# Kernel tuning notes

Measured on AMD Instinct MI355X. Metric: run time of the kernel, lower is better.

Reference implementation:

```python
import jax, jax.numpy as jnp
import numpy as np

B, N = 8, 8192
EPS = 1e-8

def _linear(x, w, b):
    return x @ w.T + b

def _block(x, w1, b1, w2, b2):
    # BlockFC: Linear -> ReLU -> Linear -> ReLU
    return jax.nn.relu(_linear(jax.nn.relu(_linear(x, w1, b1)), w2, b2))

def _transform(pc_feat, img_feat, w, b):
    # AdaIN-style: normalize point features (unbiased var, torch.var default),
    # re-modulate with per-channel image mean/std, then Linear.
    pcn = (pc_feat - pc_feat.mean(-1, keepdims=True)) / jnp.sqrt(
        jnp.var(pc_feat, axis=-1, keepdims=True, ddof=1) + EPS)
    mean = img_feat.mean((2, 3))  # [B, C]
    var = jnp.var(img_feat.reshape(img_feat.shape[0], img_feat.shape[1], -1), axis=2, ddof=1)
    out = (pcn + mean[:, None, :]) * jnp.sqrt(var[:, None, :] + EPS)
    return _linear(out, w, b)

def _project(points, feat, proj_mat):
    # Perspective projection + bilinear gather of CNN features at point locations.
    Bb, Nn, _ = points.shape
    H, W = feat.shape[2], feat.shape[3]
    p4 = jnp.concatenate([points, jnp.ones((Bb, Nn, 1), points.dtype)], -1)
    coords = jnp.einsum('bij,bnj->bni', proj_mat, p4)  # [B, N, 4]
    x = (coords[..., 0] / coords[..., 3] + 1) / 2
    y = 1 - (coords[..., 1] / coords[..., 3] + 1) / 2
    x0 = jnp.clip(x * W, 0, W - 1)
    y0 = jnp.clip(y * H, 0, H - 1)
    x1f, x2f = jnp.floor(x0), jnp.ceil(x0)
    y1f, y2f = jnp.floor(y0), jnp.ceil(y0)
    xi1, xi2 = x1f.astype(jnp.int32), x2f.astype(jnp.int32)
    yi1, yi2 = y1f.astype(jnp.int32), y2f.astype(jnp.int32)
    ft = jnp.transpose(feat, (0, 3, 2, 1))  # [B, W, H, C], matches torch transpose(1, 3)
    bidx = jnp.arange(Bb)[:, None]
    Q11 = ft[bidx, xi1, yi1]
    Q12 = ft[bidx, xi1, yi2]
    Q21 = ft[bidx, xi2, yi1]
    Q22 = ft[bidx, xi2, yi2]
    return (((x2f - x0) * (y2f - y0))[..., None] * Q11
            + ((x0 - x1f) * (y2f - y0))[..., None] * Q21
            + ((x2f - x0) * (y0 - y1f))[..., None] * Q12
            + ((x0 - x1f) * (y0 - y1f))[..., None] * Q22)

def _forward(points, feat2, feat3, feat4, feat5, proj_mat,
             b0_w1, b0_b1, b0_w2, b0_b2, t0_w, t0_b,
             b1_w1, b1_b1, b1_w2, b1_b2, t1_w, t1_b,
             b2_w1, b2_b1, b2_w2, b2_b2, t2_w, t2_b,
             b3_w1, b3_b1, b3_w2, b3_b2, t3_w, t3_b,
             d1_w, d1_b, d2_w, d2_b, d3_w, d3_b, d4_w, d4_b):
    pc0 = _block(points, b0_w1, b0_b1, b0_w2, b0_b2)   # [B, N, 64]
    f0 = _transform(pc0, feat2, t0_w, t0_b)
    pc1 = _block(pc0, b1_w1, b1_b1, b1_w2, b1_b2)      # [B, N, 128]
    f1 = _transform(pc1, feat3, t1_w, t1_b)
    pc2 = _block(pc1, b2_w1, b2_b1, b2_w2, b2_b2)      # [B, N, 256]
    f2 = _transform(pc2, feat4, t2_w, t2_b)
    pc3 = _block(pc2, b3_w1, b3_b1, b3_w2, b3_b2)      # [B, N, 512]
    f3 = _transform(pc3, feat5, t3_w, t3_b)
    feats = jnp.concatenate([
        f0, f1, f2, f3,
        _project(points, feat2, proj_mat),
        _project(points, feat3, proj_mat),
        _project(points, feat4, proj_mat),
        _project(points, feat5, proj_mat),
        points], -1)                                   # [B, N, 1923]
    x = _linear(feats, d1_w, d1_b)
    x = _linear(jax.nn.relu(x), d2_w, d2_b)
    x = _linear(jax.nn.relu(x), d3_w, d3_b)
    x = _linear(jax.nn.relu(x), d4_w, d4_b)
    return x + points

def setup_inputs() -> dict:
    key = jax.random.key(0)
    ks = iter(jax.random.split(key, 80))
    d = {}
    d['points'] = jax.random.normal(next(ks), (B, N, 3), jnp.float32)
    d['feat2'] = jax.random.normal(next(ks), (B, 64, 112, 112), jnp.float32)
    d['feat3'] = jax.random.normal(next(ks), (B, 128, 56, 56), jnp.float32)
    d['feat4'] = jax.random.normal(next(ks), (B, 256, 28, 28), jnp.float32)
    d['feat5'] = jax.random.normal(next(ks), (B, 512, 14, 14), jnp.float32)
    d['proj_mat'] = jax.random.normal(next(ks), (B, 4, 4), jnp.float32)
    def linp(wn, bn, o, i):
        d[wn] = jax.random.normal(next(ks), (o, i), jnp.float32) / np.sqrt(i)
        d[bn] = jax.random.normal(next(ks), (o,), jnp.float32) * 0.01
    linp('b0_w1', 'b0_b1', 64, 3);   linp('b0_w2', 'b0_b2', 64, 64);   linp('t0_w', 't0_b', 64, 64)
    linp('b1_w1', 'b1_b1', 128, 64); linp('b1_w2', 'b1_b2', 128, 128); linp('t1_w', 't1_b', 128, 128)
    linp('b2_w1', 'b2_b1', 256, 128);linp('b2_w2', 'b2_b2', 256, 256); linp('t2_w', 't2_b', 256, 256)
    linp('b3_w1', 'b3_b1', 512, 256);linp('b3_w2', 'b3_b2', 512, 512); linp('t3_w', 't3_b', 512, 512)
    linp('d1_w', 'd1_b', 512, 1923); linp('d2_w', 'd2_b', 256, 512)
    linp('d3_w', 'd3_b', 128, 256);  linp('d4_w', 'd4_b', 3, 128)
    return d

def reference(points, feat2, feat3, feat4, feat5, proj_mat,
              b0_w1, b0_b1, b0_w2, b0_b2, t0_w, t0_b,
              b1_w1, b1_b1, b1_w2, b1_b2, t1_w, t1_b,
              b2_w1, b2_b1, b2_w2, b2_b2, t2_w, t2_b,
              b3_w1, b3_b1, b3_w2, b3_b2, t3_w, t3_b,
              d1_w, d1_b, d2_w, d2_b, d3_w, d3_b, d4_w, d4_b):
    return _forward(points, feat2, feat3, feat4, feat5, proj_mat,
                    b0_w1, b0_b1, b0_w2, b0_b2, t0_w, t0_b,
                    b1_w1, b1_b1, b1_w2, b1_b2, t1_w, t1_b,
                    b2_w1, b2_b1, b2_w2, b2_b2, t2_w, t2_b,
                    b3_w1, b3_b1, b3_w2, b3_b2, t3_w, t3_b,
                    d1_w, d1_b, d2_w, d2_b, d3_w, d3_b, d4_w, d4_b)
```

## Files before the change

### kernel.cpp

```cpp
#include <hip/hip_runtime.h>
#include <hip/hip_bf16.h>
#include <math.h>

#define BATCH   8
#define NPTS    8192
#define MTOT    (BATCH * NPTS)
#define EPSV    1e-8f

typedef __hip_bfloat16 bf16;
typedef __attribute__((ext_vector_type(8))) short short8;
typedef __attribute__((ext_vector_type(4))) float f32x4;

__global__ __launch_bounds__(256) void stats_kernel(
    const float* __restrict__ feat, int HW,
    float* __restrict__ mean, float* __restrict__ scale)
{
    int bc = blockIdx.x;
    const float* p = feat + (size_t)bc * HW;
    float s = 0.f, s2 = 0.f;
    for (int i = threadIdx.x; i < HW; i += 256) {
        float v = p[i];
        s += v; s2 += v * v;
    }
    for (int off = 32; off; off >>= 1) {
        s  += __shfl_xor(s,  off);
        s2 += __shfl_xor(s2, off);
    }
    __shared__ float shs[4], shs2[4];
    int wave = threadIdx.x >> 6, lane = threadIdx.x & 63;
    if (lane == 0) { shs[wave] = s; shs2[wave] = s2; }
    __syncthreads();
    if (threadIdx.x == 0) {
        float S  = shs[0] + shs[1] + shs[2] + shs[3];
        float S2 = shs2[0] + shs2[1] + shs2[2] + shs2[3];
        float m = S / HW;
        float var = (S2 - HW * m * m) / (HW - 1);
        mean[bc]  = m;
        scale[bc] = sqrtf(var + EPSV);
    }
}

__global__ __launch_bounds__(256) void fold_kernel(
    const float* __restrict__ A, int lda,
    const float* __restrict__ B, int ldb,
    bf16* __restrict__ Cc, int ldc, int N, int K)
{
    __shared__ float As[16][65];
    __shared__ float Bs[16][65];
    const int tid = threadIdx.x;
    const int m0 = blockIdx.x * 64;
    const int bn = blockIdx.y * 64;
    const int tx = tid & 15, ty = tid >> 4;
    float acc[4][4] = {};

    for (int k0 = 0; k0 < K; k0 += 16) {
        #pragma unroll
        for (int i = tid; i < 64 * 16; i += 256) {
            int r = i >> 4, k = i & 15;
            As[k][r] = A[(size_t)(m0 + r) * lda + k0 + k];
        }
        #pragma unroll
        for (int i = tid; i < 64 * 16; i += 256) {
            int n = i & 63, k = i >> 6;
            Bs[k][n] = B[(size_t)(k0 + k) * ldb + bn + n];
        }
        __syncthreads();
        #pragma unroll
        for (int kk = 0; kk < 16; ++kk) {
            float a[4], b[4];
            #pragma unroll
            for (int i = 0; i < 4; ++i) a[i] = As[kk][ty * 4 + i];
            #pragma unroll
            for (int j = 0; j < 4; ++j) b[j] = Bs[kk][tx * 4 + j];
            #pragma unroll
            for (int i = 0; i < 4; ++i)
                #pragma unroll
                for (int j = 0; j < 4; ++j)
                    acc[i][j] += a[i] * b[j];
        }
        __syncthreads();
    }
    #pragma unroll
    for (int i = 0; i < 4; ++i)
        #pragma unroll
        for (int j = 0; j < 4; ++j)
            Cc[(size_t)(m0 + ty * 4 + i) * ldc + bn + tx * 4 + j] =
                __float2bfloat16(acc[i][j]);
}

__global__ __launch_bounds__(64) void bias_all(
    const float* __restrict__ d1w, const float* __restrict__ d1b,
    const float* __restrict__ t0b, const float* __restrict__ t1b,
    const float* __restrict__ t2b, const float* __restrict__ t3b,
    float* __restrict__ out)
{
    int n = blockIdx.x;
    int lane = threadIdx.x;
    const float* row = d1w + (size_t)n * 1923;
    float s = 0.f;
    for (int k = lane; k < 960; k += 64) {
        float tv;
        if (k < 64)       tv = t0b[k];
        else if (k < 192) tv = t1b[k - 64];
        else if (k < 448) tv = t2b[k - 192];
        else              tv = t3b[k - 448];
        s += row[k] * tv;
    }
    for (int off = 32; off; off >>= 1) s += __shfl_xor(s, off);
    if (lane == 0) out[n] = d1b[n] + s;
}

struct ConvDesc { const float* src; bf16* dst; int srcLd, dstLd, rows, cols; };
struct ConvArgs { ConvDesc d[20]; int n; };

__global__ __launch_bounds__(256) void conv_batch(ConvArgs a)
{
    int di = blockIdx.y;
    if (di >= a.n) return;
    ConvDesc d = a.d[di];
    int total = d.rows * d.cols;
    for (int idx = blockIdx.x * 256 + threadIdx.x; idx < total;
         idx += gridDim.x * 256) {
        int r = idx / d.cols, c = idx % d.cols;
        float v = d.src ? d.src[(size_t)r * d.srcLd + c] : 0.f;
        d.dst[(size_t)r * d.dstLd + c] = __float2bfloat16(v);
    }
}

template<int BN>
__global__ __launch_bounds__(256) void gemm_bf16(
    const bf16* __restrict__ A, int lda,
    const bf16* __restrict__ W, int ldw,
    const float* __restrict__ bias,
    bf16* __restrict__ C, int ldc,
    int gx, int gy, int K)
{
    constexpr int LDK = 40;
    __shared__ __align__(16) bf16 As[128 * LDK];
    __shared__ __align__(16) bf16 Bs[BN * LDK];

    int nblk = gx * gy;
    int bid = blockIdx.x;
    if ((nblk & 7) == 0) {
        int cpx = nblk >> 3;
        bid = (bid & 7) * cpx + (bid >> 3);
    }
    const int bm = (bid / gy) * 128;
    const int bn = (bid % gy) * BN;

    const int tid = threadIdx.x;
    const int wave = tid >> 6, lane = tid & 63;
    constexpr int FM = (BN == 128) ? 4 : 2;
    constexpr int FN = 4;
    const int wm = (BN == 128) ? (wave >> 1) * 64 : wave * 32;
    const int wn = (BN == 128) ? (wave & 1) * 64 : 0;

    f32x4 acc[FM][FN] = {};

    const int arow = tid >> 1;
    const int akh  = (tid & 1) * 16;
    const int brow = (BN == 128) ? (tid >> 1) : (tid >> 2);
    const int bkh  = (BN == 128) ? (tid & 1) * 16 : (tid & 3) * 8;

    const int fr = lane & 15, kq = lane >> 4;

    for (int k0 = 0; k0 < K; k0 += 32) {
        {
            const uint4* src = reinterpret_cast<const uint4*>(
                A + (size_t)(bm + arow) * lda + k0 + akh);
            uint4 v0 = src[0], v1 = src[1];
            uint4* dst = reinterpret_cast<uint4*>(&As[arow * LDK + akh]);
            dst[0] = v0; dst[1] = v1;
        }
        if (BN == 128) {
            const uint4* src = reinterpret_cast<const uint4*>(
                W + (size_t)(bn + brow) * ldw + k0 + bkh);
            uint4 v0 = src[0], v1 = src[1];
            uint4* dst = reinterpret_cast<uint4*>(&Bs[brow * LDK + bkh]);
            dst[0] = v0; dst[1] = v1;
        } else {
            const uint4* src = reinterpret_cast<const uint4*>(
                W + (size_t)(bn + brow) * ldw + k0 + bkh);
            uint4 v0 = src[0];
            uint4* dst = reinterpret_cast<uint4*>(&Bs[brow * LDK + bkh]);
            dst[0] = v0;
        }
        __syncthreads();

        short8 a[FM], b[FN];
        #pragma unroll
        for (int i = 0; i < FM; ++i)
            a[i] = *reinterpret_cast<const short8*>(
                &As[(wm + i * 16 + fr) * LDK + kq * 8]);
        #pragma unroll
        for (int j = 0; j < FN; ++j)
            b[j] = *reinterpret_cast<const short8*>(
                &Bs[(wn + j * 16 + fr) * LDK + kq * 8]);
        #pragma unroll
        for (int i = 0; i < FM; ++i)
            #pragma unroll
            for (int j = 0; j < FN; ++j)
                acc[i][j] = __builtin_amdgcn_mfma_f32_16x16x32_bf16(
                    a[i], b[j], acc[i][j], 0, 0, 0);
        __syncthreads();
    }

    const int rq = lane >> 4;
    #pragma unroll
    for (int j = 0; j < FN; ++j) {
        int n = bn + wn + j * 16 + fr;
        float bv = bias[n];
        #pragma unroll
        for (int i = 0; i < FM; ++i) {
            int mbase = bm + wm + i * 16 + rq * 4;
            #pragma unroll
            for (int q = 0; q < 4; ++q) {
                float v = acc[i][j][q] + bv;
                v = fmaxf(v, 0.f);
                C[(size_t)(mbase + q) * ldc + n] = __float2bfloat16(v);
            }
        }
    }
}

__global__ __launch_bounds__(256) void adain_kernel(
    const bf16* __restrict__ pc, int C, int row0,
    const float* __restrict__ img_mean, const float* __restrict__ img_scale,
    bf16* __restrict__ out, int ldout)
{
    int wave = threadIdx.x >> 6;
    int lane = threadIdx.x & 63;
    size_t row = (size_t)blockIdx.x * 4 + wave;
    int b = (int)((row0 + row) / NPTS);
    const bf16* x = pc + row * C;
    int nper = C >> 6;
    float vals[8];
    float s = 0.f, s2 = 0.f;
    for (int i = 0; i < nper; ++i) {
        float v = __bfloat162float(x[lane + (i << 6)]);
        vals[i] = v; s += v; s2 += v * v;
    }
    for (int off = 32; off; off >>= 1) {
        s  += __shfl_xor(s,  off);
        s2 += __shfl_xor(s2, off);
    }
    float mean = s / C;
    float var = (s2 - C * mean * mean) / (C - 1);
    float inv = 1.f / sqrtf(var + EPSV);
    const float* im = img_mean + (size_t)b * C;
    const float* is_ = img_scale + (size_t)b * C;
    bf16* o = out + row * ldout;
    for (int i = 0; i < nper; ++i) {
        int c = lane + (i << 6);
        o[c] = __float2bfloat16(((vals[i] - mean) * inv + im[c]) * is_[c]);
    }
}

__global__ __launch_bounds__(256) void proj_kernel(
    const float* __restrict__ points, const float* __restrict__ pm,
    const float* __restrict__ feat, int C, int H, int W, int row0, int Mc,
    bf16* __restrict__ out, int ldout)
{
    size_t idx = (size_t)blockIdx.x * 256 + threadIdx.x;
    size_t total = (size_t)Mc * C;
    if (idx >= total) return;
    int c = (int)(idx % C);
    size_t m = idx / C;
    size_t gm = (size_t)row0 + m;
    int b = (int)(gm / NPTS);
    const float* p = points + gm * 3;
    const float* P = pm + (size_t)b * 16;
    float px = p[0], py = p[1], pz = p[2];
    float c0 = P[0]  * px + P[1]  * py + P[2]  * pz + P[3];
    float c1 = P[4]  * px + P[5]  * py + P[6]  * pz + P[7];
    float c3 = P[12] * px + P[13] * py + P[14] * pz + P[15];
    float x = (c0 / c3 + 1.f) * 0.5f;
    float y = 1.f - (c1 / c3 + 1.f) * 0.5f;
    float x0 = fminf(fmaxf(x * W, 0.f), (float)(W - 1));
    float y0 = fminf(fmaxf(y * H, 0.f), (float)(H - 1));
    float x1f = floorf(x0), x2f = ceilf(x0);
    float y1f = floorf(y0), y2f = ceilf(y0);
    int xi1 = (int)x1f, xi2 = (int)x2f, yi1 = (int)y1f, yi2 = (int)y2f;
    const float* fb = feat + ((size_t)b * C + c) * (size_t)(H * W);
    float Q11 = fb[yi1 * W + xi1];
    float Q12 = fb[yi2 * W + xi1];
    float Q21 = fb[yi1 * W + xi2];
    float Q22 = fb[yi2 * W + xi2];
    float wx2 = x2f - x0, wx1 = x0 - x1f;
    float wy2 = y2f - y0, wy1 = y0 - y1f;
    float r = wx2 * wy2 * Q11 + wx1 * wy2 * Q21
            + wx2 * wy1 * Q12 + wx1 * wy1 * Q22;
    out[m * ldout + c] = __float2bfloat16(r);
}

__global__ __launch_bounds__(256) void copy3_kernel(
    const float* __restrict__ pts, int row0, int Mc,
    bf16* __restrict__ dst, int dld)
{
    int m = blockIdx.x * 256 + threadIdx.x;
    if (m >= Mc) return;
    const float* p = pts + (size_t)(row0 + m) * 3;
    bf16* d = dst + (size_t)m * dld;
    d[0] = __float2bfloat16(p[0]);
    d[1] = __float2bfloat16(p[1]);
    d[2] = __float2bfloat16(p[2]);
}

__global__ __launch_bounds__(256) void final_kernel(
    const bf16* __restrict__ x3, const float* __restrict__ w,
    const float* __restrict__ bb, const float* __restrict__ points,
    int row0, int Mc, float* __restrict__ out)
{
    size_t m = (size_t)blockIdx.x * 256 + threadIdx.x;
    if (m >= (size_t)Mc) return;
    size_t gm = (size_t)row0 + m;
    float a0 = bb[0], a1 = bb[1], a2 = bb[2];
    const bf16* x = x3 + m * 128;
    #pragma unroll 4
    for (int k = 0; k < 128; ++k) {
        float v = __bfloat162float(x[k]);
        a0 += v * w[k];
        a1 += v * w[128 + k];
        a2 += v * w[256 + k];
    }
    out[gm * 3 + 0] = a0 + points[gm * 3 + 0];
    out[gm * 3 + 1] = a1 + points[gm * 3 + 1];
    out[gm * 3 + 2] = a2 + points[gm * 3 + 2];
}

extern "C" void kernel_launch(void* const* d_in, const int* in_sizes, int n_in,
                              void* d_out, int out_size, void* d_ws, size_t ws_size,
                              hipStream_t stream)
{
    const float* points = (const float*)d_in[0];
    const float* feat2  = (const float*)d_in[1];
    const float* feat3  = (const float*)d_in[2];
    const float* feat4  = (const float*)d_in[3];
    const float* feat5  = (const float*)d_in[4];
    const float* pmat   = (const float*)d_in[5];
    const float* b0w1 = (const float*)d_in[6];  const float* b0b1 = (const float*)d_in[7];
    const float* b0w2 = (const float*)d_in[8];  const float* b0b2 = (const float*)d_in[9];
    const float* t0w  = (const float*)d_in[10]; const float* t0b  = (const float*)d_in[11];
    const float* b1w1 = (const float*)d_in[12]; const float* b1b1 = (const float*)d_in[13];
    const float* b1w2 = (const float*)d_in[14]; const float* b1b2 = (const float*)d_in[15];
    const float* t1w  = (const float*)d_in[16]; const float* t1b  = (const float*)d_in[17];
    const float* b2w1 = (const float*)d_in[18]; const float* b2b1 = (const float*)d_in[19];
    const float* b2w2 = (const float*)d_in[20]; const float* b2b2 = (const float*)d_in[21];
    const float* t2w  = (const float*)d_in[22]; const float* t2b  = (const float*)d_in[23];
    const float* b3w1 = (const float*)d_in[24]; const float* b3b1 = (const float*)d_in[25];
    const float* b3w2 = (const float*)d_in[26]; const float* b3b2 = (const float*)d_in[27];
    const float* t3w  = (const float*)d_in[28]; const float* t3b  = (const float*)d_in[29];
    const float* d1w  = (const float*)d_in[30]; const float* d1b  = (const float*)d_in[31];
    const float* d2w  = (const float*)d_in[32]; const float* d2b  = (const float*)d_in[33];
    const float* d3w  = (const float*)d_in[34]; const float* d3b  = (const float*)d_in[35];
    const float* d4w  = (const float*)d_in[36]; const float* d4b  = (const float*)d_in[37];

    float* wsf = (float*)d_ws;
    float* biasTot = wsf;
    float* smean   = wsf + 512;
    float* sscale  = smean + 7680;
    const size_t F32_FLOATS = 512 + 2 * 7680;
    float* mean2 = smean, *mean3 = smean + 512, *mean4 = smean + 1536, *mean5 = smean + 3584;
    float* scl2 = sscale, *scl3 = sscale + 512, *scl4 = sscale + 1536, *scl5 = sscale + 3584;

    bf16* wb = (bf16*)(wsf + F32_FLOATS);
    bf16* Wd1   = wb;
    bf16* b0w1p = Wd1   + (size_t)512 * 1952;
    bf16* b0w2b = b0w1p + 64 * 32;
    bf16* b1w1b = b0w2b + 64 * 64;
    bf16* b1w2b = b1w1b + 128 * 64;
    bf16* b2w1b = b1w2b + 128 * 128;
    bf16* b2w2b = b2w1b + 256 * 128;
    bf16* b3w1b = b2w2b + 256 * 256;
    bf16* b3w2b = b3w1b + 512 * 256;
    bf16* d2wb  = b3w2b + (size_t)512 * 512;
    bf16* d3wb  = d2wb  + (size_t)256 * 512;
    const size_t SHARED_BF = (size_t)512 * 1952 + 64 * 32 + 64 * 64 + 128 * 64
        + 128 * 128 + 256 * 128 + 256 * 256 + (size_t)512 * 256
        + (size_t)512 * 512 + (size_t)256 * 512 + 128 * 256;

    const size_t SHARED_BYTES = F32_FLOATS * 4 + SHARED_BF * 2;

    const size_t PER_ROW_BYTES = 4352 * 2;
    size_t avail = (ws_size > SHARED_BYTES) ? ws_size - SHARED_BYTES : 0;
    int nch = 1;
    while (nch < 512 && (size_t)(MTOT / nch) * PER_ROW_BYTES > avail) nch <<= 1;
    const int Mc = MTOT / nch;

    bf16* cb = wb + SHARED_BF;
    bf16* ptsb  = cb;
    bf16* hbuf  = ptsb  + (size_t)Mc * 32;
    bf16* pc0   = hbuf  + (size_t)Mc * 512;
    bf16* pc1   = pc0   + (size_t)Mc * 64;
    bf16* pc2   = pc1   + (size_t)Mc * 128;
    bf16* pc3   = pc2   + (size_t)Mc * 256;
    bf16* feats = pc3   + (size_t)Mc * 512;
    bf16* x1r   = feats + (size_t)Mc * 1952;
    bf16* x2    = x1r   + (size_t)Mc * 512;
    bf16* x3    = x2    + (size_t)Mc * 256;

    stats_kernel<<<8 * 64,  256, 0, stream>>>(feat2, 112 * 112, mean2, scl2);
    stats_kernel<<<8 * 128, 256, 0, stream>>>(feat3, 56 * 56,  mean3, scl3);
    stats_kernel<<<8 * 256, 256, 0, stream>>>(feat4, 28 * 28,  mean4, scl4);
    stats_kernel<<<8 * 512, 256, 0, stream>>>(feat5, 14 * 14,  mean5, scl5);

    ConvArgs ca;
    int nd = 0;
    auto addc = [&](const float* s, bf16* d, int sld, int dld, int r, int c) {
        ca.d[nd++] = ConvDesc{ s, d, sld, dld, r, c };
    };
    addc(b0w1, b0w1p, 3, 32, 64, 3);
    addc(nullptr, b0w1p + 3, 0, 32, 64, 29);
    addc(b0w2, b0w2b, 64, 64, 64, 64);
    addc(b1w1, b1w1b, 64, 64, 128, 64);
    addc(b1w2, b1w2b, 128, 128, 128, 128);
    addc(b2w1, b2w1b, 128, 128, 256, 128);
    addc(b2w2, b2w2b, 256, 256, 256, 256);
    addc(b3w1, b3w1b, 256, 256, 512, 256);
    addc(b3w2, b3w2b, 512, 512, 512, 512);
    addc(d2w, d2wb, 512, 512, 256, 512);
    addc(d3w, d3wb, 256, 256, 128, 256);
    addc(d1w + 960,  Wd1 + 960,  1923, 1952, 512, 64);
    addc(d1w + 1024, Wd1 + 1024, 1923, 1952, 512, 128);
    addc(d1w + 1152, Wd1 + 1152, 1923, 1952, 512, 256);
    addc(d1w + 1408, Wd1 + 1408, 1923, 1952, 512, 512);
    addc(d1w + 1920, Wd1 + 1920, 1923, 1952, 512, 3);
    addc(nullptr,    Wd1 + 1923, 0,    1952, 512, 29);
    ca.n = nd;
    conv_batch<<<dim3(64, nd), 256, 0, stream>>>(ca);

    fold_kernel<<<dim3(8, 1), 256, 0, stream>>>(d1w + 0,   1923, t0w, 64,  Wd1 + 0,   1952, 64,  64);
    fold_kernel<<<dim3(8, 2), 256, 0, stream>>>(d1w + 64,  1923, t1w, 128, Wd1 + 64,  1952, 128, 128);
    fold_kernel<<<dim3(8, 4), 256, 0, stream>>>(d1w + 192, 1923, t2w, 256, Wd1 + 192, 1952, 256, 256);
    fold_kernel<<<dim3(8, 8), 256, 0, stream>>>(d1w + 448, 1923, t3w, 512, Wd1 + 448, 1952, 512, 512);
    bias_all<<<512, 64, 0, stream>>>(d1w, d1b, t0b, t1b, t2b, t3b, biasTot);

    auto G = [&](const bf16* A, int lda, const bf16* Wt, int ldw,
                 const float* bias, bf16* Cout, int ldc, int N, int K) {
        if (N >= 128) {
            int gy = N / 128, gx = Mc / 128;
            gemm_bf16<128><<<gx * gy, 256, 0, stream>>>(A, lda, Wt, ldw, bias,
                                                        Cout, ldc, gx, gy, K);
        } else {
            int gy = N / 64, gx = Mc / 128;
            gemm_bf16<64><<<gx * gy, 256, 0, stream>>>(A, lda, Wt, ldw, bias,
                                                       Cout, ldc, gx, gy, K);
        }
    };

    for (int ch = 0; ch < nch; ++ch) {
        const int row0 = ch * Mc;

        copy3_kernel<<<(Mc + 255) / 256, 256, 0, stream>>>(points, row0, Mc, ptsb, 32);

        G(ptsb, 32, b0w1p, 32, b0b1, hbuf, 64, 64, 32);
        G(hbuf, 64, b0w2b, 64, b0b2, pc0, 64, 64, 64);
        adain_kernel<<<Mc / 4, 256, 0, stream>>>(pc0, 64, row0, mean2, scl2, feats + 0, 1952);
        G(pc0, 64, b1w1b, 64, b1b1, hbuf, 128, 128, 64);
        G(hbuf, 128, b1w2b, 128, b1b2, pc1, 128, 128, 128);
        adain_kernel<<<Mc / 4, 256, 0, stream>>>(pc1, 128, row0, mean3, scl3, feats + 64, 1952);
        G(pc1, 128, b2w1b, 128, b2b1, hbuf, 256, 256, 128);
        G(hbuf, 256, b2w2b, 256, b2b2, pc2, 256, 256, 256);
        adain_kernel<<<Mc / 4, 256, 0, stream>>>(pc2, 256, row0, mean4, scl4, feats + 192, 1952);
        G(pc2, 256, b3w1b, 256, b3b1, hbuf, 512, 512, 256);
        G(hbuf, 512, b3w2b, 512, b3b2, pc3, 512, 512, 512);
        adain_kernel<<<Mc / 4, 256, 0, stream>>>(pc3, 512, row0, mean5, scl5, feats + 448, 1952);

        size_t tot;
        tot = (size_t)Mc * 64;
        proj_kernel<<<(tot + 255) / 256, 256, 0, stream>>>(points, pmat, feat2, 64, 112, 112, row0, Mc, feats + 960, 1952);
        tot = (size_t)Mc * 128;
        proj_kernel<<<(tot + 255) / 256, 256, 0, stream>>>(points, pmat, feat3, 128, 56, 56, row0, Mc, feats + 1024, 1952);
        tot = (size_t)Mc * 256;
        proj_kernel<<<(tot + 255) / 256, 256, 0, stream>>>(points, pmat, feat4, 256, 28, 28, row0, Mc, feats + 1152, 1952);
        tot = (size_t)Mc * 512;
        proj_kernel<<<(tot + 255) / 256, 256, 0, stream>>>(points, pmat, feat5, 512, 14, 14, row0, Mc, feats + 1408, 1952);

        copy3_kernel<<<(Mc + 255) / 256, 256, 0, stream>>>(points, row0, Mc, feats + 1920, 1952);

        G(feats, 1952, Wd1, 1952, biasTot, x1r, 512, 512, 1952);
        G(x1r, 512, d2wb, 512, d2b, x2, 256, 256, 512);
        G(x2, 256, d3wb, 256, d3b, x3, 128, 128, 256);
        final_kernel<<<(Mc + 255) / 256, 256, 0, stream>>>(x3, d4w, d4b, points,
                                                           row0, Mc, (float*)d_out);
    }
}
```

Measured before the change: 1.777 ms.

## Merge weight-fold GEMMs into one split-K launch with a reduction kernel

```diff
diff --git a/kernel.cpp b/kernel.cpp
--- a/kernel.cpp
+++ b/kernel.cpp
@@ -40,29 +40,40 @@
     }
 }
 
-__global__ __launch_bounds__(256) void fold_kernel(
-    const float* __restrict__ A, int lda,
-    const float* __restrict__ B, int ldb,
-    bf16* __restrict__ Cc, int ldc, int N, int K)
-{
+struct FoldDesc { int aoff; const float* B; int C; int nbase; int blkBase; int nt; int kt; };
+struct FoldArgs { FoldDesc d[4]; };
+
+__global__ __launch_bounds__(256) void fold_splitk(
+    const float* __restrict__ d1w, float* __restrict__ foldtmp, FoldArgs args)
+{
+    int bid = blockIdx.x;
+    int f = (bid >= 168) ? 3 : (bid >= 40) ? 2 : (bid >= 8) ? 1 : 0;
+    FoldDesc d = args.d[f];
+    int local = bid - d.blkBase;
+    int ks  = local % d.kt;
+    int ntI = (local / d.kt) % d.nt;
+    int mt  = local / (d.kt * d.nt);
+    const int m0 = mt * 64, n0 = ntI * 64, kbase = ks * 64;
+
+    const float* A = d1w + d.aoff;
+    const float* B = d.B;
+
     __shared__ float As[16][65];
     __shared__ float Bs[16][65];
     const int tid = threadIdx.x;
-    const int m0 = blockIdx.x * 64;
-    const int bn = blockIdx.y * 64;
     const int tx = tid & 15, ty = tid >> 4;
     float acc[4][4] = {};
 
-    for (int k0 = 0; k0 < K; k0 += 16) {
+    for (int k0 = kbase; k0 < kbase + 64; k0 += 16) {
         #pragma unroll
         for (int i = tid; i < 64 * 16; i += 256) {
             int r = i >> 4, k = i & 15;
-            As[k][r] = A[(size_t)(m0 + r) * lda + k0 + k];
+            As[k][r] = A[(size_t)(m0 + r) * 1923 + k0 + k];
         }
         #pragma unroll
         for (int i = tid; i < 64 * 16; i += 256) {
             int n = i & 63, k = i >> 6;
-            Bs[k][n] = B[(size_t)(k0 + k) * ldb + bn + n];
+            Bs[k][n] = B[(size_t)(k0 + k) * d.C + n0 + n];
         }
         __syncthreads();
         #pragma unroll
@@ -80,12 +91,26 @@
         }
         __syncthreads();
     }
+    float* dst = foldtmp + ((size_t)ks * 512) * 960;
     #pragma unroll
     for (int i = 0; i < 4; ++i)
         #pragma unroll
         for (int j = 0; j < 4; ++j)
-            Cc[(size_t)(m0 + ty * 4 + i) * ldc + bn + tx * 4 + j] =
-                __float2bfloat16(acc[i][j]);
+            dst[(size_t)(m0 + ty * 4 + i) * 960 + d.nbase + n0 + tx * 4 + j] =
+                acc[i][j];
+}
+
+__global__ __launch_bounds__(256) void fold_convert(
+    const float* __restrict__ foldtmp, bf16* __restrict__ Wd1)
+{
+    int idx = blockIdx.x * 256 + threadIdx.x;
+    if (idx >= 512 * 960) return;
+    int m = idx / 960, n = idx % 960;
+    int kt = (n < 64) ? 1 : (n < 192) ? 2 : (n < 448) ? 4 : 8;
+    float s = 0.f;
+    for (int k = 0; k < kt; ++k)
+        s += foldtmp[((size_t)k * 512 + m) * 960 + n];
+    Wd1[(size_t)m * 1952 + n] = __float2bfloat16(s);
 }
 
 __global__ __launch_bounds__(64) void bias_all(
@@ -359,7 +384,8 @@
     float* biasTot = wsf;
     float* smean   = wsf + 512;
     float* sscale  = smean + 7680;
-    const size_t F32_FLOATS = 512 + 2 * 7680;
+    float* foldtmp = sscale + 7680;
+    const size_t F32_FLOATS = 512 + 2 * 7680 + (size_t)8 * 512 * 960;
     float* mean2 = smean, *mean3 = smean + 512, *mean4 = smean + 1536, *mean5 = smean + 3584;
     float* scl2 = sscale, *scl3 = sscale + 512, *scl4 = sscale + 1536, *scl5 = sscale + 3584;
 
@@ -429,10 +455,13 @@
     ca.n = nd;
     conv_batch<<<dim3(64, nd), 256, 0, stream>>>(ca);
 
-    fold_kernel<<<dim3(8, 1), 256, 0, stream>>>(d1w + 0,   1923, t0w, 64,  Wd1 + 0,   1952, 64,  64);
-    fold_kernel<<<dim3(8, 2), 256, 0, stream>>>(d1w + 64,  1923, t1w, 128, Wd1 + 64,  1952, 128, 128);
-    fold_kernel<<<dim3(8, 4), 256, 0, stream>>>(d1w + 192, 1923, t2w, 256, Wd1 + 192, 1952, 256, 256);
-    fold_kernel<<<dim3(8, 8), 256, 0, stream>>>(d1w + 448, 1923, t3w, 512, Wd1 + 448, 1952, 512, 512);
+    FoldArgs fa;
+    fa.d[0] = FoldDesc{ 0,   t0w, 64,  0,   0,   1, 1 };
+    fa.d[1] = FoldDesc{ 64,  t1w, 128, 64,  8,   2, 2 };
+    fa.d[2] = FoldDesc{ 192, t2w, 256, 192, 40,  4, 4 };
+    fa.d[3] = FoldDesc{ 448, t3w, 512, 448, 168, 8, 8 };
+    fold_splitk<<<680, 256, 0, stream>>>(d1w, foldtmp, fa);
+    fold_convert<<<(512 * 960 + 255) / 256, 256, 0, stream>>>(foldtmp, Wd1);
     bias_all<<<512, 64, 0, stream>>>(d1w, d1b, t0b, t1b, t2b, t3b, biasTot);
 
     auto G = [&](const bf16* A, int lda, const bf16* Wt, int ldw,
```

New measurement: 1.626 ms. -8.5%, faster.
